# Performance work log

Measured on AMD Instinct MI355X. Metric: run time of the kernel, lower is better.

Reference implementation:

```python
import jax, jax.numpy as jnp
import numpy as np

D = 1024
N_HEADS = 16
D_HEAD = D // N_HEADS
D_FF = 4096
EPS = 1e-5


def setup_inputs() -> dict:
    key = jax.random.key(0)
    ks = jax.random.split(key, 9)
    s = 0.02
    x = jax.random.normal(ks[0], (4, 2048, D), dtype=jnp.float32)
    Wq = jax.random.normal(ks[1], (D, D), dtype=jnp.float32) * s
    Wk = jax.random.normal(ks[2], (D, D), dtype=jnp.float32) * s
    Wv = jax.random.normal(ks[3], (D, D), dtype=jnp.float32) * s
    Wo = jax.random.normal(ks[4], (D, D), dtype=jnp.float32) * s
    W1 = jax.random.normal(ks[5], (D, D_FF), dtype=jnp.float32) * s
    W2 = jax.random.normal(ks[6], (D_FF, D), dtype=jnp.float32) * s
    g1 = jnp.ones((D,), dtype=jnp.float32)
    g2 = jnp.ones((D,), dtype=jnp.float32)
    return {"x": x, "Wq": Wq, "Wk": Wk, "Wv": Wv, "Wo": Wo,
            "W1": W1, "W2": W2, "g1": g1, "g2": g2}


def rmsnorm(x, g):
    rms = jnp.sqrt(jnp.mean(x * x, axis=-1, keepdims=True) + EPS)
    return x / rms * g


def attention(x, Wq, Wk, Wv, Wo):
    B, T, C = x.shape
    q = (x @ Wq).reshape(B, T, N_HEADS, D_HEAD).transpose(0, 2, 1, 3)  # [B,H,T,dh]
    k = (x @ Wk).reshape(B, T, N_HEADS, D_HEAD).transpose(0, 2, 1, 3)
    v = (x @ Wv).reshape(B, T, N_HEADS, D_HEAD).transpose(0, 2, 1, 3)
    att = jnp.einsum("bhqd,bhkd->bhqk", q, k) * (D_HEAD ** -0.5)
    causal = jnp.tril(jnp.ones((T, T), dtype=bool))
    att = jnp.where(causal, att, -jnp.inf)
    att = jax.nn.softmax(att, axis=-1)
    y = jnp.einsum("bhqk,bhkd->bhqd", att, v)
    y = y.transpose(0, 2, 1, 3).reshape(B, T, C)
    return y @ Wo


def reference(x, Wq, Wk, Wv, Wo, W1, W2, g1, g2):
    x = x + attention(rmsnorm(x, g1), Wq, Wk, Wv, Wo)
    h = rmsnorm(x, g2)
    x = x + (jax.nn.gelu(h @ W1, approximate=False) @ W2)
    return x
```

## Files before the change

### kernel.cpp

```cpp
#include <hip/hip_runtime.h>
#include <hip/hip_bf16.h>


typedef __attribute__((ext_vector_type(8))) short bf16x8;
typedef __attribute__((ext_vector_type(4))) float f32x4;
typedef __attribute__((ext_vector_type(8))) unsigned short u16x8;
typedef __attribute__((ext_vector_type(4))) unsigned short u16x4;

#define DEV static __device__ __forceinline__

DEV unsigned short f2b(float f){
  __hip_bfloat16 h = __float2bfloat16(f);
  union { __hip_bfloat16 h; unsigned short u; } cv; cv.h = h; return cv.u;
}

DEV void async16(const void* g, void* l){
  __builtin_amdgcn_global_load_lds((__attribute__((address_space(1))) void*)(void*)g,
                                   (__attribute__((address_space(3))) void*)l, 16, 0, 0);
}

__global__ __launch_bounds__(256) void transpose_bf16(
    const float* __restrict__ in, unsigned short* __restrict__ out, int R, int C)
{
  __shared__ float tile[32][33];
  int c0 = blockIdx.x * 32, r0 = blockIdx.y * 32;
  int tx = threadIdx.x & 31, ty = threadIdx.x >> 5;
#pragma unroll
  for (int i = 0; i < 4; i++)
    tile[ty + 8*i][tx] = in[(size_t)(r0 + ty + 8*i) * C + c0 + tx];
  __syncthreads();
#pragma unroll
  for (int i = 0; i < 4; i++)
    out[(size_t)(c0 + ty + 8*i) * R + r0 + tx] = f2b(tile[tx][ty + 8*i]);
}

__global__ __launch_bounds__(256) void rmsnorm_k(
    const float* __restrict__ x, const float* __restrict__ g,
    unsigned short* __restrict__ out)
{
  int row = blockIdx.x, t = threadIdx.x;
  const float4* xr = (const float4*)(x + (size_t)row * 1024);
  float4 v = xr[t];
  float ss = v.x*v.x + v.y*v.y + v.z*v.z + v.w*v.w;
#pragma unroll
  for (int o = 32; o > 0; o >>= 1) ss += __shfl_xor(ss, o, 64);
  __shared__ float wsum[4];
  int lane = t & 63, wv = t >> 6;
  if (lane == 0) wsum[wv] = ss;
  __syncthreads();
  float inv = rsqrtf((wsum[0]+wsum[1]+wsum[2]+wsum[3]) * (1.0f/1024.0f) + 1e-5f);
  float4 gv = ((const float4*)g)[t];
  u16x4 o;
  o[0] = f2b(v.x * inv * gv.x);
  o[1] = f2b(v.y * inv * gv.y);
  o[2] = f2b(v.z * inv * gv.z);
  o[3] = f2b(v.w * inv * gv.w);
  *(u16x4*)(out + (size_t)row * 1024 + t * 4) = o;
}

template<int MODE>
__global__ __launch_bounds__(256) void gemm_bt(
    const unsigned short* __restrict__ A,
    const unsigned short* __restrict__ Bt,
    const float* __restrict__ resid,
    float* __restrict__ outF,
    unsigned short* __restrict__ outB,
    int N, int K)
{
  __shared__ __attribute__((aligned(16))) unsigned short lA[128*64];
  __shared__ __attribute__((aligned(16))) unsigned short lB[128*64];

  const int nTn = N >> 7;
  const int nwg = gridDim.x;
  int wg = ((int)blockIdx.x & 7) * (nwg >> 3) + ((int)blockIdx.x >> 3);
  const int tm = wg / nTn, tn = wg % nTn;
  const int tid = threadIdx.x;
  const int lane = tid & 63, w = tid >> 6;
  const int r15 = lane & 15, hi = lane >> 4;
  const int wm = (w >> 1) << 6, wn = (w & 1) << 6;

  f32x4 acc[4][4];
#pragma unroll
  for (int i = 0; i < 4; i++)
#pragma unroll
    for (int j = 0; j < 4; j++) acc[i][j] = f32x4{0.f, 0.f, 0.f, 0.f};

  const size_t arow0 = (size_t)tm * 128;
  const size_t brow0 = (size_t)tn * 128;

  for (int k0 = 0; k0 < K; k0 += 64) {
    __syncthreads();
#pragma unroll
    for (int i = 0; i < 4; i++) {
      int s = (i*4 + w) * 64 + lane;
      int row = s >> 3, sl = s & 7;
      int col = (sl ^ (row & 7)) << 3;
      async16(A + (arow0 + row) * K + k0 + col, (char*)lA + (size_t)(i*4 + w) * 1024);
    }
#pragma unroll
    for (int i = 0; i < 4; i++) {
      int s = (i*4 + w) * 64 + lane;
      int row = s >> 3, sl = s & 7;
      int col = (sl ^ (row & 7)) << 3;
      async16(Bt + (brow0 + row) * K + k0 + col, (char*)lB + (size_t)(i*4 + w) * 1024);
    }
    __syncthreads();

#pragma unroll
    for (int kc = 0; kc < 2; kc++) {
      bf16x8 af[4], bfr[4];
#pragma unroll
      for (int mi = 0; mi < 4; mi++) {
        int row = wm + mi*16 + r15;
        int esl = (kc*4 + hi) ^ (row & 7);
        af[mi] = *(const bf16x8*)&lA[row*64 + esl*8];
      }
#pragma unroll
      for (int ni = 0; ni < 4; ni++) {
        int row = wn + ni*16 + r15;
        int esl = (kc*4 + hi) ^ (row & 7);
        bfr[ni] = *(const bf16x8*)&lB[row*64 + esl*8];
      }
#pragma unroll
      for (int mi = 0; mi < 4; mi++)
#pragma unroll
        for (int ni = 0; ni < 4; ni++)
          acc[mi][ni] = __builtin_amdgcn_mfma_f32_16x16x32_bf16(
              af[mi], bfr[ni], acc[mi][ni], 0, 0, 0);
    }
  }

#pragma unroll
  for (int mi = 0; mi < 4; mi++) {
#pragma unroll
    for (int ni = 0; ni < 4; ni++) {
#pragma unroll
      for (int r = 0; r < 4; r++) {
        size_t row = arow0 + wm + mi*16 + hi*4 + r;
        size_t col = brow0 + wn + ni*16 + r15;
        size_t idx = row * (size_t)N + col;
        float v = acc[mi][ni][r];
        if (MODE == 0)      outB[idx] = f2b(v);
        else if (MODE == 1) outF[idx] = v + resid[idx];
        else if (MODE == 2) outB[idx] = f2b(0.5f * v * (1.0f + erff(v * 0.70710678118654752f)));
        else                outF[idx] = v + resid[idx];
      }
    }
  }
}

__global__ __launch_bounds__(256) void attn_k(
    const unsigned short* __restrict__ QKV, unsigned short* __restrict__ outB)
{
  const int nwg = gridDim.x;
  int logical = ((int)blockIdx.x & 7) * (nwg >> 3) + ((int)blockIdx.x >> 3);
  int qt = 31 - (logical & 31);
  int bh = logical >> 5;
  int b = bh >> 4, h = bh & 15;
  const int tid = threadIdx.x, lane = tid & 63, w = tid >> 6;
  const int r15 = lane & 15, hi = lane >> 4;
  const int LD = 3072;
  const size_t rowbase = (size_t)b * 2048;
  const int q0 = qt * 64;
  const int qw = q0 + w * 16;
  const int myq = qw + r15;

  bf16x8 aq[2];
  {
    const unsigned short* qp = QKV + (rowbase + myq) * LD + h * 64;
    aq[0] = *(const bf16x8*)(qp + hi * 8);
    aq[1] = *(const bf16x8*)(qp + 32 + hi * 8);
  }

  __shared__ __attribute__((aligned(16))) unsigned short lK[64 * 64];
  __shared__ __attribute__((aligned(16))) unsigned short lVt[64 * 72];
  __shared__ __attribute__((aligned(16))) unsigned short lP[4][16 * 64];

  f32x4 y[4];
#pragma unroll
  for (int db = 0; db < 4; db++) y[db] = f32x4{0.f, 0.f, 0.f, 0.f};
  float mrow = -1e30f, lrow = 0.f;

  const int nkt = qt + 1;
  const float SC = 0.18033688011112042f;

  const int krow0 = w*8 + (lane >> 3);
  const int kch   = lane & 7;

  for (int kt = 0; kt < nkt; kt++) {
    const int kb = kt * 64;
    __syncthreads();
#pragma unroll
    for (int i = 0; i < 2; i++) {
      int row = krow0 + i*32;
      int col = (kch ^ (row & 7)) * 8;
      async16(QKV + (rowbase + kb + row) * LD + 1024 + h*64 + col,
              (char*)lK + (size_t)(i*4 + w) * 1024);
    }
#pragma unroll
    for (int i = 0; i < 2; i++) {
      int row = krow0 + i*32;
      const unsigned short* vp = QKV + (rowbase + kb + row) * LD + 2048 + h*64 + kch*8;
      u16x8 vv = *(const u16x8*)vp;
      int vbase = (kch*8)*72 + (row ^ (kch*8));
#pragma unroll
      for (int j = 0; j < 8; j++)
        lVt[vbase + j*72] = vv[j];
    }
    __syncthreads();

    f32x4 s[4];
#pragma unroll
    for (int tb = 0; tb < 4; tb++) s[tb] = f32x4{0.f, 0.f, 0.f, 0.f};
#pragma unroll
    for (int tb = 0; tb < 4; tb++) {
      int krow = tb*16 + r15;
#pragma unroll
      for (int kc = 0; kc < 2; kc++) {
        bf16x8 kf = *(const bf16x8*)&lK[krow*64 + ((kc*4 + hi) ^ (krow & 7))*8];
        s[tb] = __builtin_amdgcn_mfma_f32_16x16x32_bf16(kf, aq[kc], s[tb], 0, 0, 0);
      }
    }

    if (kb + 63 > qw) {
#pragma unroll
      for (int tb = 0; tb < 4; tb++)
#pragma unroll
        for (int r = 0; r < 4; r++)
          if (kb + tb*16 + hi*4 + r > myq) s[tb][r] = -1e30f;
    }

    float mx = -1e30f;
#pragma unroll
    for (int tb = 0; tb < 4; tb++)
#pragma unroll
      for (int r = 0; r < 4; r++) mx = fmaxf(mx, s[tb][r]);
    mx = fmaxf(mx, __shfl_xor(mx, 16, 64));
    mx = fmaxf(mx, __shfl_xor(mx, 32, 64));
    float mnew = fmaxf(mrow, mx);
    float m2 = mnew * SC;
    float al = __builtin_amdgcn_exp2f(fmaf(mrow, SC, -m2));
    mrow = mnew;

    unsigned short* lPw = &lP[w][0];
    const int prot = 8 * (r15 & 7);
    float rs = 0.f;
#pragma unroll
    for (int tb = 0; tb < 4; tb++) {
      float p0 = __builtin_amdgcn_exp2f(fmaf(s[tb][0], SC, -m2));
      float p1 = __builtin_amdgcn_exp2f(fmaf(s[tb][1], SC, -m2));
      float p2 = __builtin_amdgcn_exp2f(fmaf(s[tb][2], SC, -m2));
      float p3 = __builtin_amdgcn_exp2f(fmaf(s[tb][3], SC, -m2));
      rs += (p0 + p1) + (p2 + p3);
      u16x4 pk;
      pk[0] = f2b(p0); pk[1] = f2b(p1); pk[2] = f2b(p2); pk[3] = f2b(p3);
      *(u16x4*)&lPw[r15*64 + ((tb*16 + hi*4) ^ prot)] = pk;
    }
    rs += __shfl_xor(rs, 16, 64);
    rs += __shfl_xor(rs, 32, 64);
    lrow = lrow * al + rs;
#pragma unroll
    for (int db = 0; db < 4; db++)
#pragma unroll
      for (int r = 0; r < 4; r++) y[db][r] *= al;

    asm volatile("s_waitcnt lgkmcnt(0)" ::: "memory");
    __builtin_amdgcn_sched_barrier(0);

#pragma unroll
    for (int kc2 = 0; kc2 < 2; kc2++) {
      bf16x8 pf = *(const bf16x8*)&lPw[r15*64 + ((kc2*32 + hi*8) ^ prot)];
#pragma unroll
      for (int db = 0; db < 4; db++) {
        int d = db*16 + r15;
        bf16x8 vf = *(const bf16x8*)&lVt[d*72 + ((kc2*32 + hi*8) ^ (d & 56))];
        y[db] = __builtin_amdgcn_mfma_f32_16x16x32_bf16(vf, pf, y[db], 0, 0, 0);
      }
    }
  }

  float inv = 1.0f / lrow;
  const size_t obase = (rowbase + myq) * 1024 + h*64;
#pragma unroll
  for (int db = 0; db < 4; db++) {
    u16x4 o;
#pragma unroll
    for (int r = 0; r < 4; r++) o[r] = f2b(y[db][r] * inv);
    *(u16x4*)(outB + obase + db*16 + hi*4) = o;
  }
}

extern "C" void kernel_launch(void* const* d_in, const int* in_sizes, int n_in,
                              void* d_out, int out_size, void* d_ws, size_t ws_size,
                              hipStream_t stream) {
  const float* x  = (const float*)d_in[0];
  const float* Wq = (const float*)d_in[1];
  const float* Wk = (const float*)d_in[2];
  const float* Wv = (const float*)d_in[3];
  const float* Wo = (const float*)d_in[4];
  const float* W1 = (const float*)d_in[5];
  const float* W2 = (const float*)d_in[6];
  const float* g1 = (const float*)d_in[7];
  const float* g2 = (const float*)d_in[8];
  float* out = (float*)d_out;

  unsigned short* wQKVt = (unsigned short*)d_ws;
  unsigned short* wOt   = wQKVt + (size_t)3072 * 1024;
  unsigned short* w1t   = wOt   + (size_t)1024 * 1024;
  unsigned short* w2t   = w1t   + (size_t)4096 * 1024;
  unsigned short* xn    = w2t   + (size_t)1024 * 4096;
  unsigned short* attno = xn    + (size_t)8192 * 1024;
  unsigned short* qkv   = attno + (size_t)8192 * 1024;
  unsigned short* hff   = attno;

  transpose_bf16<<<dim3(32, 32),  256, 0, stream>>>(Wq, wQKVt,                     1024, 1024);
  transpose_bf16<<<dim3(32, 32),  256, 0, stream>>>(Wk, wQKVt + (size_t)1024*1024, 1024, 1024);
  transpose_bf16<<<dim3(32, 32),  256, 0, stream>>>(Wv, wQKVt + (size_t)2048*1024, 1024, 1024);
  transpose_bf16<<<dim3(32, 32),  256, 0, stream>>>(Wo, wOt,                       1024, 1024);
  transpose_bf16<<<dim3(128, 32), 256, 0, stream>>>(W1, w1t,                       1024, 4096);
  transpose_bf16<<<dim3(32, 128), 256, 0, stream>>>(W2, w2t,                       4096, 1024);

  rmsnorm_k<<<8192, 256, 0, stream>>>(x, g1, xn);
  gemm_bt<0><<<64 * 24, 256, 0, stream>>>(xn, wQKVt, nullptr, nullptr, qkv, 3072, 1024);
  attn_k<<<2048, 256, 0, stream>>>(qkv, attno);
  gemm_bt<1><<<64 * 8, 256, 0, stream>>>(attno, wOt, x, out, nullptr, 1024, 1024);
  rmsnorm_k<<<8192, 256, 0, stream>>>(out, g2, xn);
  gemm_bt<2><<<64 * 32, 256, 0, stream>>>(xn, w1t, nullptr, nullptr, hff, 4096, 1024);
  gemm_bt<3><<<64 * 8, 256, 0, stream>>>(hff, w2t, out, out, nullptr, 1024, 4096);
}
```

Measured before the change: 532.8 us.

## Double-buffer GEMM LDS tiles and enlarge tiles to 256-wide with 8 waves

The GEMM kernel now uses two LDS buffers, so the async global-to-LDS load of the next K-slice is issued while MFMAs run on the current one. This replaces the two barriers per iteration with one. Tile sizes become templated (256x256 or 128x256) with 512 threads and launch_bounds(512,1), which raises per-workgroup data reuse. The cost is fewer workgroups (256 to 512 per GEMM on a 256-CU part) and higher register and LDS pressure: up to 128KB of LDS for the 256x256 tiles, which may limit occupancy or fail to fit.

```diff
diff --git a/kernel.cpp b/kernel.cpp
--- a/kernel.cpp
+++ b/kernel.cpp
@@ -58,8 +58,8 @@
   *(u16x4*)(out + (size_t)row * 1024 + t * 4) = o;
 }
 
-template<int MODE>
-__global__ __launch_bounds__(256) void gemm_bt(
+template<int BM, int BN, int MODE>
+__global__ __launch_bounds__(512, 1) void gemm_bt(
     const unsigned short* __restrict__ A,
     const unsigned short* __restrict__ Bt,
     const float* __restrict__ resid,
@@ -67,71 +67,81 @@
     unsigned short* __restrict__ outB,
     int N, int K)
 {
-  __shared__ __attribute__((aligned(16))) unsigned short lA[128*64];
-  __shared__ __attribute__((aligned(16))) unsigned short lB[128*64];
-
-  const int nTn = N >> 7;
+  constexpr int MR = BM / 32;
+  constexpr int NA = BM / 64;
+  constexpr int NB = BN / 64;
+  __shared__ __attribute__((aligned(16))) unsigned short lA[2][BM*64];
+  __shared__ __attribute__((aligned(16))) unsigned short lB[2][BN*64];
+
+  const int nTn = N / BN;
   const int nwg = gridDim.x;
   int wg = ((int)blockIdx.x & 7) * (nwg >> 3) + ((int)blockIdx.x >> 3);
   const int tm = wg / nTn, tn = wg % nTn;
   const int tid = threadIdx.x;
   const int lane = tid & 63, w = tid >> 6;
   const int r15 = lane & 15, hi = lane >> 4;
-  const int wm = (w >> 1) << 6, wn = (w & 1) << 6;
-
-  f32x4 acc[4][4];
-#pragma unroll
-  for (int i = 0; i < 4; i++)
+  const int wm = (w >> 2) * (BM/2), wn = (w & 3) * 64;
+
+  f32x4 acc[MR][4];
+#pragma unroll
+  for (int i = 0; i < MR; i++)
 #pragma unroll
     for (int j = 0; j < 4; j++) acc[i][j] = f32x4{0.f, 0.f, 0.f, 0.f};
 
-  const size_t arow0 = (size_t)tm * 128;
-  const size_t brow0 = (size_t)tn * 128;
+  const size_t arow0 = (size_t)tm * BM;
+  const size_t brow0 = (size_t)tn * BN;
+  const int srow = lane >> 3, sch = lane & 7;
+
+  auto stage = [&](int buf, int k0) {
+#pragma unroll
+    for (int i = 0; i < NA; i++) {
+      int slot = i*8 + w;
+      int row = slot*8 + srow;
+      int col = (sch ^ (row & 7)) << 3;
+      async16(A + (arow0 + row) * K + k0 + col,
+              (char*)&lA[buf][0] + (size_t)slot * 1024);
+    }
+#pragma unroll
+    for (int i = 0; i < NB; i++) {
+      int slot = i*8 + w;
+      int row = slot*8 + srow;
+      int col = (sch ^ (row & 7)) << 3;
+      async16(Bt + (brow0 + row) * K + k0 + col,
+              (char*)&lB[buf][0] + (size_t)slot * 1024);
+    }
+  };
+
+  int cur = 0;
+  stage(0, 0);
+  __syncthreads();
 
   for (int k0 = 0; k0 < K; k0 += 64) {
-    __syncthreads();
-#pragma unroll
-    for (int i = 0; i < 4; i++) {
-      int s = (i*4 + w) * 64 + lane;
-      int row = s >> 3, sl = s & 7;
-      int col = (sl ^ (row & 7)) << 3;
-      async16(A + (arow0 + row) * K + k0 + col, (char*)lA + (size_t)(i*4 + w) * 1024);
-    }
-#pragma unroll
-    for (int i = 0; i < 4; i++) {
-      int s = (i*4 + w) * 64 + lane;
-      int row = s >> 3, sl = s & 7;
-      int col = (sl ^ (row & 7)) << 3;
-      async16(Bt + (brow0 + row) * K + k0 + col, (char*)lB + (size_t)(i*4 + w) * 1024);
-    }
-    __syncthreads();
+    if (k0 + 64 < K) stage(cur ^ 1, k0 + 64);
 
 #pragma unroll
     for (int kc = 0; kc < 2; kc++) {
-      bf16x8 af[4], bfr[4];
-#pragma unroll
-      for (int mi = 0; mi < 4; mi++) {
-        int row = wm + mi*16 + r15;
-        int esl = (kc*4 + hi) ^ (row & 7);
-        af[mi] = *(const bf16x8*)&lA[row*64 + esl*8];
-      }
+      bf16x8 bfr[4];
 #pragma unroll
       for (int ni = 0; ni < 4; ni++) {
         int row = wn + ni*16 + r15;
-        int esl = (kc*4 + hi) ^ (row & 7);
-        bfr[ni] = *(const bf16x8*)&lB[row*64 + esl*8];
-      }
-#pragma unroll
-      for (int mi = 0; mi < 4; mi++)
+        bfr[ni] = *(const bf16x8*)&lB[cur][row*64 + (((kc*4 + hi) ^ (row & 7)) << 3)];
+      }
+#pragma unroll
+      for (int mi = 0; mi < MR; mi++) {
+        int row = wm + mi*16 + r15;
+        bf16x8 af = *(const bf16x8*)&lA[cur][row*64 + (((kc*4 + hi) ^ (row & 7)) << 3)];
 #pragma unroll
         for (int ni = 0; ni < 4; ni++)
           acc[mi][ni] = __builtin_amdgcn_mfma_f32_16x16x32_bf16(
-              af[mi], bfr[ni], acc[mi][ni], 0, 0, 0);
-    }
-  }
-
-#pragma unroll
-  for (int mi = 0; mi < 4; mi++) {
+              af, bfr[ni], acc[mi][ni], 0, 0, 0);
+      }
+    }
+    __syncthreads();
+    cur ^= 1;
+  }
+
+#pragma unroll
+  for (int mi = 0; mi < MR; mi++) {
 #pragma unroll
     for (int ni = 0; ni < 4; ni++) {
 #pragma unroll
@@ -321,10 +331,10 @@
   transpose_bf16<<<dim3(32, 128), 256, 0, stream>>>(W2, w2t,                       4096, 1024);
 
   rmsnorm_k<<<8192, 256, 0, stream>>>(x, g1, xn);
-  gemm_bt<0><<<64 * 24, 256, 0, stream>>>(xn, wQKVt, nullptr, nullptr, qkv, 3072, 1024);
+  gemm_bt<256,256,0><<<32 * 12, 512, 0, stream>>>(xn, wQKVt, nullptr, nullptr, qkv, 3072, 1024);
   attn_k<<<2048, 256, 0, stream>>>(qkv, attno);
-  gemm_bt<1><<<64 * 8, 256, 0, stream>>>(attno, wOt, x, out, nullptr, 1024, 1024);
+  gemm_bt<128,256,1><<<64 * 4, 512, 0, stream>>>(attno, wOt, x, out, nullptr, 1024, 1024);
   rmsnorm_k<<<8192, 256, 0, stream>>>(out, g2, xn);
-  gemm_bt<2><<<64 * 32, 256, 0, stream>>>(xn, w1t, nullptr, nullptr, hff, 4096, 1024);
-  gemm_bt<3><<<64 * 8, 256, 0, stream>>>(hff, w2t, out, out, nullptr, 1024, 4096);
-}
+  gemm_bt<256,256,2><<<32 * 16, 512, 0, stream>>>(xn, w1t, nullptr, nullptr, hff, 4096, 1024);
+  gemm_bt<128,256,3><<<64 * 4, 512, 0, stream>>>(hff, w2t, out, out, nullptr, 1024, 4096);
+}
```

After: 532.5 us. Within noise of the previous version (-0.1%).
